# Performance work log

Measured on AMD Instinct MI355X. Metric: run time of the kernel, lower is better.

## Reference

```python
import jax, jax.numpy as jnp
import numpy as np

D_MODEL = 1024
NHEAD = 16
HEAD_DIM = D_MODEL // NHEAD
LN_EPS = 1e-5


def setup_inputs() -> dict:
    key = jax.random.key(0)
    ks = jax.random.split(key, 6)
    B, S = 4, 4096
    x = jax.random.normal(ks[0], (B, S, D_MODEL), dtype=jnp.float32)
    scale = 0.02
    Wq = jax.random.normal(ks[1], (D_MODEL, D_MODEL), dtype=jnp.float32) * scale
    Wv = jax.random.normal(ks[2], (D_MODEL, D_MODEL), dtype=jnp.float32) * scale
    Wo = jax.random.normal(ks[3], (D_MODEL, D_MODEL), dtype=jnp.float32) * scale
    Wg = jax.random.normal(ks[4], (D_MODEL, D_MODEL), dtype=jnp.float32) * scale
    beta = jnp.full((NHEAD,), -0.2, dtype=jnp.float32)
    ln_gamma = jnp.ones((D_MODEL,), dtype=jnp.float32)
    ln_beta = jnp.zeros((D_MODEL,), dtype=jnp.float32)
    return {"x": x, "Wq": Wq, "Wv": Wv, "Wo": Wo, "Wg": Wg,
            "beta": beta, "ln_gamma": ln_gamma, "ln_beta": ln_beta}


def _ema_scan(lam, v):
    # v: [B, S, H, D]; lam: [1, 1, H, 1]
    # s_t = lam * s_{t-1} + v_t, computed with a parallel associative scan
    # on pairs (a, b) representing the affine map s -> a*s + b.
    a = jnp.broadcast_to(lam, v.shape)

    def combine(e1, e2):
        a1, b1 = e1
        a2, b2 = e2
        return a1 * a2, a2 * b1 + b2

    _, state = jax.lax.associative_scan(combine, (a, v), axis=1)
    return state


def reference(x, Wq, Wv, Wo, Wg, beta, ln_gamma, ln_beta):
    B, S, _ = x.shape
    q = (x @ Wq.T).reshape(B, S, NHEAD, HEAD_DIM)
    v = (x @ Wv.T).reshape(B, S, NHEAD, HEAD_DIM)
    lam = jax.nn.sigmoid(beta).reshape(1, 1, NHEAD, 1).astype(v.dtype)
    state = _ema_scan(lam, v)                      # [B, S, H, D]
    y = (q * state).reshape(B, S, D_MODEL)
    # LayerNorm over last dim
    mu = jnp.mean(y, axis=-1, keepdims=True)
    var = jnp.mean(jnp.square(y - mu), axis=-1, keepdims=True)
    y = (y - mu) * jax.lax.rsqrt(var + LN_EPS) * ln_gamma + ln_beta
    gate = jax.nn.silu(x @ Wg.T)
    y = y * gate
    return y @ Wo.T
```

## Files before the change

kernel.cpp:

```cpp
#include <hip/hip_runtime.h>

#define D_MODEL 1024
#define NHEAD 16
#define LN_EPS 1e-5f
#define CHUNK 32
#define S_LEN 4096
#define NCH (S_LEN / CHUNK)

typedef unsigned short u16;
typedef __attribute__((ext_vector_type(8))) short short8;
typedef __attribute__((ext_vector_type(8))) unsigned short u16x8;
typedef __attribute__((ext_vector_type(4))) float f32x4;

__device__ __forceinline__ u16 f2b(float f) {
  unsigned u = __builtin_bit_cast(unsigned, f);
  u += 0x7FFFu + ((u >> 16) & 1u);
  return (u16)(u >> 16);
}
__device__ __forceinline__ float b2f(u16 s) {
  return __builtin_bit_cast(float, ((unsigned)s) << 16);
}

__device__ __forceinline__ ushort4 cvt4(float4 f) {
  ushort4 o; o.x = f2b(f.x); o.y = f2b(f.y); o.z = f2b(f.z); o.w = f2b(f.w);
  return o;
}
__global__ __launch_bounds__(256) void cvt_all(
    const float4* __restrict__ x,  const float4* __restrict__ wq,
    const float4* __restrict__ wv, const float4* __restrict__ wg,
    const float4* __restrict__ wo, ushort4* __restrict__ xb,
    ushort4* __restrict__ wqvg, ushort4* __restrict__ wob,
    const float* __restrict__ beta, float* __restrict__ lam,
    int nx4, int nw4) {
  int i = blockIdx.x * blockDim.x + threadIdx.x;
  int stride = gridDim.x * blockDim.x;
  if (blockIdx.x == 0 && threadIdx.x < NHEAD) {
    float l = 1.f / (1.f + __expf(-beta[threadIdx.x]));
    lam[threadIdx.x] = l;
    lam[NHEAD + threadIdx.x] = __log2f(l);
  }
  for (int j = i; j < nx4; j += stride) xb[j] = cvt4(x[j]);
  for (int j = i; j < nw4; j += stride) wqvg[j] = cvt4(wq[j]);
  for (int j = i; j < nw4; j += stride) wqvg[nw4 + j] = cvt4(wv[j]);
  for (int j = i; j < nw4; j += stride) wqvg[2 * nw4 + j] = cvt4(wg[j]);
  for (int j = i; j < nw4; j += stride) wob[j] = cvt4(wo[j]);
}


__device__ __forceinline__ void glds16(const u16* g, const u16* l) {
  __builtin_amdgcn_global_load_lds(
      (const __attribute__((address_space(1))) unsigned*)g,
      (__attribute__((address_space(3))) unsigned*)l, 16, 0, 0);
}

#define BAR() asm volatile("s_barrier" ::: "memory")
#define SB0() __builtin_amdgcn_sched_barrier(0)

template <typename OutT, bool CARRY>
__global__ __launch_bounds__(512, 2) void gemm256(const u16* __restrict__ X,
                                                  const u16* __restrict__ W,
                                                  OutT* __restrict__ Out,
                                                  float* __restrict__ carry,
                                                  const float* __restrict__ lamlog,
                                                  int M, int N, int K) {
  __shared__ u16 sm[8][8192];
  const int tid = threadIdx.x;
  const int lane = tid & 63;
  const int wave = tid >> 6;
  const int ln15 = lane & 15, lh = lane >> 4;
  const int wr = wave >> 2, wc = wave & 3;
  const int bm = blockIdx.x * 256, bn = blockIdx.y * 256;
  const int NT = K >> 6;

  const int srow = tid >> 3;
  const int scol = ((tid & 7) ^ (srow & 7)) << 3;
  const u16* Asrc = X + (size_t)(bm + srow) * K + scol;
  const u16* Bsrc = W + (size_t)(bn + srow) * K + scol;
  const int ldsw = wave * 512;

#define STAGE(u, h, tile, src)                                          \
  { const u16* _g = (src) + (size_t)((h) * 128) * K + (tile) * 64;      \
    glds16(_g,                  &sm[u][ldsw]);                          \
    glds16(_g + (size_t)64 * K, &sm[u][ldsw + 4096]); }

  const char* smb = (const char*)&sm[0][0];
  const char* Ard = smb + wr * 16384 + ln15 * 128;
  const char* Brd = smb + (2 + (wc >> 1)) * 16384 + ((wc & 1) * 64 + ln15) * 128;
  const int swz0 = ((lh ^ (ln15 & 7)) << 4);
  const int swz1 = (((4 + lh) ^ (ln15 & 7)) << 4);

#define RD_A(DB, MM, S) (*(const short8*)(Ard + (DB) + (MM) * 2048 + (S)))
#define RD_B(DB, NN, S) (*(const short8*)(Brd + (DB) + (NN) * 2048 + (S)))

  f32x4 acc[8][4];
  f32x4 zero = {0.f, 0.f, 0.f, 0.f};
  #pragma unroll
  for (int m = 0; m < 8; ++m)
    #pragma unroll
    for (int n = 0; n < 4; ++n) acc[m][n] = zero;

  short8 a[8][2], b[4][2];

#define MFMA_Q(M0, N0)                                                        \
  SB0();                                                                      \
  __builtin_amdgcn_s_setprio(1);                                              \
  _Pragma("unroll")                                                           \
  for (int m = (M0); m < (M0) + 4; ++m)                                       \
    _Pragma("unroll")                                                         \
    for (int n = (N0); n < (N0) + 2; ++n) {                                   \
      acc[m][n] = __builtin_amdgcn_mfma_f32_16x16x32_bf16(a[m][0], b[n][0], acc[m][n], 0, 0, 0); \
      acc[m][n] = __builtin_amdgcn_mfma_f32_16x16x32_bf16(a[m][1], b[n][1], acc[m][n], 0, 0, 0); \
    }                                                                         \
  __builtin_amdgcn_s_setprio(0);                                              \
  SB0();

  STAGE(0, 0, 0, Asrc); STAGE(1, 1, 0, Asrc);
  STAGE(2, 0, 0, Bsrc); STAGE(3, 1, 0, Bsrc);
  STAGE(4, 0, 1, Asrc); STAGE(5, 1, 1, Asrc);
  asm volatile("s_waitcnt vmcnt(4)" ::: "memory");
  BAR();
  #pragma unroll
  for (int m = 0; m < 4; ++m) { a[m][0] = RD_A(0, m, swz0); a[m][1] = RD_A(0, m, swz1); }
  #pragma unroll
  for (int n = 0; n < 4; ++n) { b[n][0] = RD_B(0, n, swz0); b[n][1] = RD_B(0, n, swz1); }

  for (int t = 0; t < NT; ++t) {
    const int d = t & 1;
    const int db = d * 65536;
    const int odb = (d ^ 1) * 65536;
    const int od = (d ^ 1) * 4;
    const int sd = d * 4;
    const int tB = (t + 1 < NT) ? t + 1 : NT - 1;
    const int tA = (t + 2 < NT) ? t + 2 : NT - 1;

    a[4][0] = RD_A(db, 4, swz0); a[4][1] = RD_A(db, 4, swz1);
    a[5][0] = RD_A(db, 5, swz0); a[5][1] = RD_A(db, 5, swz1);
    STAGE(od + 2, 0, tB, Bsrc);
    MFMA_Q(0, 0)

    a[6][0] = RD_A(db, 6, swz0); a[6][1] = RD_A(db, 6, swz1);
    a[7][0] = RD_A(db, 7, swz0); a[7][1] = RD_A(db, 7, swz1);
    STAGE(od + 3, 1, tB, Bsrc);
    MFMA_Q(0, 2)
    asm volatile("s_waitcnt vmcnt(4)" ::: "memory");
    BAR();

    #pragma unroll
    for (int m = 0; m < 4; ++m) { a[m][0] = RD_A(odb, m, swz0); a[m][1] = RD_A(odb, m, swz1); }
    MFMA_Q(4, 2)
    STAGE(sd + 0, 0, tA, Asrc);
    asm volatile("s_waitcnt vmcnt(2)" ::: "memory");
    BAR();

    b[2][0] = RD_B(odb, 2, swz0); b[2][1] = RD_B(odb, 2, swz1);
    b[3][0] = RD_B(odb, 3, swz0); b[3][1] = RD_B(odb, 3, swz1);
    MFMA_Q(4, 0)
    b[0][0] = RD_B(odb, 0, swz0); b[0][1] = RD_B(odb, 0, swz1);
    b[1][0] = RD_B(odb, 1, swz0); b[1][1] = RD_B(odb, 1, swz1);
    STAGE(sd + 1, 1, tA, Asrc);
  }
#undef STAGE
#undef RD_A
#undef RD_B
#undef MFMA_Q

  if constexpr (CARRY) {
    if (bn >= 1024 && bn < 2048) {
      const float l2h = lamlog[((bn - 1024) + wc * 64) >> 6];
      const float lp1 = exp2f(l2h);
      const float lp2 = lp1 * lp1, lp3 = lp2 * lp1, lp4 = lp2 * lp2;
      const float l8 = lp4 * lp4;
      const float lpl = exp2f(l2h * (float)(4 * lh));
      #pragma unroll
      for (int q = 0; q < 4; ++q)
        #pragma unroll
        for (int n = 0; n < 4; ++n) {
          f32x4 A0 = acc[2 * q][n], A1 = acc[2 * q + 1][n];
          A0[1] += lp1 * A0[0]; A0[2] += lp1 * A0[1]; A0[3] += lp1 * A0[2];
          A1[1] += lp1 * A1[0]; A1[2] += lp1 * A1[1]; A1[3] += lp1 * A1[2];
          float S = A0[3], x;
          x = __shfl_up(S, 16); if (lh >= 1) S += lp4 * x;
          x = __shfl_up(S, 32); if (lh >= 2) S += l8 * x;
          float Xc = __shfl_up(S, 16); Xc = (lh >= 1) ? Xc : 0.f;
          A0[0] += lp1 * Xc; A0[1] += lp2 * Xc; A0[2] += lp3 * Xc; A0[3] += lp4 * Xc;
          float f15 = __shfl(A0[3], 48 + ln15);
          S = A1[3];
          x = __shfl_up(S, 16); if (lh >= 1) S += lp4 * x;
          x = __shfl_up(S, 32); if (lh >= 2) S += l8 * x;
          Xc = __shfl_up(S, 16); Xc = (lh >= 1) ? Xc : 0.f;
          Xc += lpl * f15;
          A1[0] += lp1 * Xc; A1[1] += lp2 * Xc; A1[2] += lp3 * Xc; A1[3] += lp4 * Xc;
          acc[2 * q][n] = A0; acc[2 * q + 1][n] = A1;
        }
    }
  }

  #pragma unroll
  for (int m = 0; m < 8; ++m)
    #pragma unroll
    for (int n = 0; n < 4; ++n)
      #pragma unroll
      for (int r = 0; r < 4; ++r) {
        int row = bm + wr * 128 + m * 16 + lh * 4 + r;
        int col = bn + wc * 64 + n * 16 + ln15;
        float vv = acc[m][n][r];
        if constexpr (sizeof(OutT) == 2) Out[(size_t)row * N + col] = f2b(vv);
        else                             Out[(size_t)row * N + col] = vv;
      }

  if constexpr (CARRY) {
    if (bn >= 1024 && bn < 2048 && lh == 3) {
      const int bidx = bm >> 12;
      const int chunkbase = ((bm & 4095) >> 5) + wr * 4;
      const int colbase = (bn - 1024) + wc * 64;
      #pragma unroll
      for (int q = 0; q < 4; ++q)
        #pragma unroll
        for (int n = 0; n < 4; ++n)
          carry[(size_t)(bidx * NCH + chunkbase + q) * D_MODEL +
                colbase + n * 16 + ln15] = acc[2 * q + 1][n][3];
    }
  }
}

__global__ void scan_carry(float* __restrict__ carry, const float* __restrict__ lam,
                           int B, int nch) {
  int idx = blockIdx.x * blockDim.x + threadIdx.x;
  if (idx >= B * D_MODEL) return;
  int b = idx >> 10, col = idx & (D_MODEL - 1);
  float lC = exp2f(lam[NHEAD + (col >> 6)] * (float)CHUNK);
  float c = 0.f;
  #pragma unroll 4
  for (int j = 0; j < nch; ++j) {
    size_t a = ((size_t)(b * nch + j)) * D_MODEL + col;
    c = lC * c + carry[a];
    carry[a] = c;
  }
}

__global__ __launch_bounds__(256) void ew_ln(const u16* __restrict__ qvg,
    const float* __restrict__ carry, const float* __restrict__ lam,
    const float* __restrict__ gamma, const float* __restrict__ lbeta,
    u16* __restrict__ yout, int nch, int ld) {
  const int wave = threadIdx.x >> 6;
  const int lane = threadIdx.x & 63;
  const int row = blockIdx.x * 4 + wave;
  const int b = row >> 12;
  const int srow = row & 4095;
  const int j = srow >> 5, tl = srow & 31;
  const int col0 = lane * 16;
  const size_t rb = (size_t)row * ld;

  u16x8 qu0 = *(const u16x8*)(qvg + rb + col0);
  u16x8 qu1 = *(const u16x8*)(qvg + rb + col0 + 8);
  u16x8 su0 = *(const u16x8*)(qvg + rb + D_MODEL + col0);
  u16x8 su1 = *(const u16x8*)(qvg + rb + D_MODEL + col0 + 8);
  u16x8 gu0 = *(const u16x8*)(qvg + rb + 2 * D_MODEL + col0);
  u16x8 gu1 = *(const u16x8*)(qvg + rb + 2 * D_MODEL + col0 + 8);

  float st[16];
  #pragma unroll
  for (int i = 0; i < 8; ++i) { st[i] = b2f(su0[i]); st[8 + i] = b2f(su1[i]); }
  if (j > 0) {
    float p = exp2f(lam[NHEAD + (col0 >> 6)] * (float)(tl + 1));
    const float* cb = carry + ((size_t)(b * nch + j - 1)) * D_MODEL + col0;
    const float4 c0 = *(const float4*)(cb);
    const float4 c1 = *(const float4*)(cb + 4);
    const float4 c2 = *(const float4*)(cb + 8);
    const float4 c3 = *(const float4*)(cb + 12);
    st[0]  += p * c0.x; st[1]  += p * c0.y; st[2]  += p * c0.z; st[3]  += p * c0.w;
    st[4]  += p * c1.x; st[5]  += p * c1.y; st[6]  += p * c1.z; st[7]  += p * c1.w;
    st[8]  += p * c2.x; st[9]  += p * c2.y; st[10] += p * c2.z; st[11] += p * c2.w;
    st[12] += p * c3.x; st[13] += p * c3.y; st[14] += p * c3.z; st[15] += p * c3.w;
  }
  float y[16];
  float sum = 0.f, sumsq = 0.f;
  #pragma unroll
  for (int i = 0; i < 8; ++i) {
    y[i] = b2f(qu0[i]) * st[i];
    y[8 + i] = b2f(qu1[i]) * st[8 + i];
  }
  #pragma unroll
  for (int i = 0; i < 16; ++i) { sum += y[i]; sumsq += y[i] * y[i]; }
  #pragma unroll
  for (int off = 32; off > 0; off >>= 1) {
    sum += __shfl_xor(sum, off);
    sumsq += __shfl_xor(sumsq, off);
  }
  const float mu = sum * (1.f / 1024.f);
  const float var = sumsq * (1.f / 1024.f) - mu * mu;
  const float rstd = rsqrtf(var + LN_EPS);

  u16x8 o0, o1;
  #pragma unroll
  for (int i = 0; i < 8; ++i) {
    float gm = gamma[col0 + i], bt = lbeta[col0 + i];
    float g = b2f(gu0[i]);
    o0[i] = f2b(((y[i] - mu) * rstd * gm + bt) * (g / (1.f + __expf(-g))));
    gm = gamma[col0 + 8 + i]; bt = lbeta[col0 + 8 + i];
    g = b2f(gu1[i]);
    o1[i] = f2b(((y[8 + i] - mu) * rstd * gm + bt) * (g / (1.f + __expf(-g))));
  }
  *(u16x8*)(yout + (size_t)row * D_MODEL + col0) = o0;
  *(u16x8*)(yout + (size_t)row * D_MODEL + col0 + 8) = o1;
}

extern "C" void kernel_launch(void* const* d_in, const int* in_sizes, int n_in,
                              void* d_out, int out_size, void* d_ws, size_t ws_size,
                              hipStream_t stream) {
  const float* x     = (const float*)d_in[0];
  const float* Wq    = (const float*)d_in[1];
  const float* Wv    = (const float*)d_in[2];
  const float* Wo    = (const float*)d_in[3];
  const float* Wg    = (const float*)d_in[4];
  const float* beta  = (const float*)d_in[5];
  const float* gamma = (const float*)d_in[6];
  const float* lbeta = (const float*)d_in[7];
  float* out = (float*)d_out;

  const int BS = in_sizes[0] / D_MODEL;
  const int B = BS / S_LEN;
  const int nch = NCH;
  const size_t nx = (size_t)BS * D_MODEL;
  const size_t nw = (size_t)D_MODEL * D_MODEL;
  const int N3 = 3 * D_MODEL;

  char* w = (char*)d_ws;
  u16* xb   = (u16*)w;  w += nx * 2;
  u16* wqvg = (u16*)w;  w += 3 * nw * 2;
  u16* wob  = (u16*)w;  w += nw * 2;
  u16* qvg  = (u16*)w;  w += (size_t)BS * N3 * 2;
  u16* yb   = (u16*)w;  w += nx * 2;
  float* carry = (float*)w;  w += (size_t)B * nch * D_MODEL * 4;
  float* lam = (float*)w;

  cvt_all<<<2048, 256, 0, stream>>>((const float4*)x, (const float4*)Wq,
      (const float4*)Wv, (const float4*)Wg, (const float4*)Wo,
      (ushort4*)xb, (ushort4*)wqvg, (ushort4*)wob, beta, lam,
      (int)(nx / 4), (int)(nw / 4));

  dim3 g1(BS / 256, N3 / 256);
  gemm256<u16, true><<<g1, 512, 0, stream>>>(xb, wqvg, qvg, carry, lam + NHEAD,
                                             BS, N3, D_MODEL);

  scan_carry<<<(B * D_MODEL + 255) / 256, 256, 0, stream>>>(carry, lam, B, nch);
  ew_ln<<<BS / 4, 256, 0, stream>>>(qvg, carry, lam, gamma, lbeta, yb, nch, N3);

  dim3 g2(BS / 256, D_MODEL / 256);
  gemm256<float, false><<<g2, 512, 0, stream>>>(yb, wob, out, nullptr, nullptr,
                                                BS, D_MODEL, D_MODEL);
}
```

Baseline: 222.9 us.

## Load GEMM B operand directly from global into registers, halve LDS

The B (weight) tile is no longer staged through LDS. Each wave now reads its B fragments straight from global memory into double-buffered registers (bE/bO), and only the A tile is staged in LDS, which shrinks shared memory from 128KB to 64KB. The main loop is unrolled by two to alternate register buffers, and the waitcnt/barrier schedule is reworked to match. This removes LDS traffic and barriers for B and frees LDS for occupancy, at the cost of redundant uncoalesced global/L2 reads of B across waves and higher register pressure.

```diff
diff --git a/kernel.cpp b/kernel.cpp
--- a/kernel.cpp
+++ b/kernel.cpp
@@ -63,7 +63,7 @@
                                                   float* __restrict__ carry,
                                                   const float* __restrict__ lamlog,
                                                   int M, int N, int K) {
-  __shared__ u16 sm[8][8192];
+  __shared__ u16 sm[4][8192];
   const int tid = threadIdx.x;
   const int lane = tid & 63;
   const int wave = tid >> 6;
@@ -75,22 +75,27 @@
   const int srow = tid >> 3;
   const int scol = ((tid & 7) ^ (srow & 7)) << 3;
   const u16* Asrc = X + (size_t)(bm + srow) * K + scol;
-  const u16* Bsrc = W + (size_t)(bn + srow) * K + scol;
   const int ldsw = wave * 512;
 
-#define STAGE(u, h, tile, src)                                          \
-  { const u16* _g = (src) + (size_t)((h) * 128) * K + (tile) * 64;      \
+#define STAGE_A(u, h, tile)                                             \
+  { const u16* _g = Asrc + (size_t)((h) * 128) * K + (tile) * 64;       \
     glds16(_g,                  &sm[u][ldsw]);                          \
     glds16(_g + (size_t)64 * K, &sm[u][ldsw + 4096]); }
 
+  const u16* Bgl = W + (size_t)(bn + wc * 64 + ln15) * K + lh * 8;
+#define LOADB(BV, tile)                                                 \
+  _Pragma("unroll")                                                     \
+  for (int n = 0; n < 4; ++n) {                                         \
+    BV[n][0] = *(const short8*)(Bgl + (size_t)n * 16 * K + (tile) * 64);      \
+    BV[n][1] = *(const short8*)(Bgl + (size_t)n * 16 * K + (tile) * 64 + 32); \
+  }
+
   const char* smb = (const char*)&sm[0][0];
   const char* Ard = smb + wr * 16384 + ln15 * 128;
-  const char* Brd = smb + (2 + (wc >> 1)) * 16384 + ((wc & 1) * 64 + ln15) * 128;
   const int swz0 = ((lh ^ (ln15 & 7)) << 4);
   const int swz1 = (((4 + lh) ^ (ln15 & 7)) << 4);
 
 #define RD_A(DB, MM, S) (*(const short8*)(Ard + (DB) + (MM) * 2048 + (S)))
-#define RD_B(DB, NN, S) (*(const short8*)(Brd + (DB) + (NN) * 2048 + (S)))
 
   f32x4 acc[8][4];
   f32x4 zero = {0.f, 0.f, 0.f, 0.f};
@@ -99,69 +104,73 @@
     #pragma unroll
     for (int n = 0; n < 4; ++n) acc[m][n] = zero;
 
-  short8 a[8][2], b[4][2];
-
-#define MFMA_Q(M0, N0)                                                        \
+  short8 a[8][2], bE[4][2], bO[4][2];
+
+#define MFMA_Q(M0, N0, BV)                                                    \
   SB0();                                                                      \
   __builtin_amdgcn_s_setprio(1);                                              \
   _Pragma("unroll")                                                           \
   for (int m = (M0); m < (M0) + 4; ++m)                                       \
     _Pragma("unroll")                                                         \
     for (int n = (N0); n < (N0) + 2; ++n) {                                   \
-      acc[m][n] = __builtin_amdgcn_mfma_f32_16x16x32_bf16(a[m][0], b[n][0], acc[m][n], 0, 0, 0); \
-      acc[m][n] = __builtin_amdgcn_mfma_f32_16x16x32_bf16(a[m][1], b[n][1], acc[m][n], 0, 0, 0); \
+      acc[m][n] = __builtin_amdgcn_mfma_f32_16x16x32_bf16(a[m][0], BV[n][0], acc[m][n], 0, 0, 0); \
+      acc[m][n] = __builtin_amdgcn_mfma_f32_16x16x32_bf16(a[m][1], BV[n][1], acc[m][n], 0, 0, 0); \
     }                                                                         \
   __builtin_amdgcn_s_setprio(0);                                              \
   SB0();
 
-  STAGE(0, 0, 0, Asrc); STAGE(1, 1, 0, Asrc);
-  STAGE(2, 0, 0, Bsrc); STAGE(3, 1, 0, Bsrc);
-  STAGE(4, 0, 1, Asrc); STAGE(5, 1, 1, Asrc);
+  LOADB(bE, 0)
+  STAGE_A(0, 0, 0) STAGE_A(1, 1, 0)
+  STAGE_A(2, 0, 1) STAGE_A(3, 1, 1)
   asm volatile("s_waitcnt vmcnt(4)" ::: "memory");
   BAR();
   #pragma unroll
   for (int m = 0; m < 4; ++m) { a[m][0] = RD_A(0, m, swz0); a[m][1] = RD_A(0, m, swz1); }
-  #pragma unroll
-  for (int n = 0; n < 4; ++n) { b[n][0] = RD_B(0, n, swz0); b[n][1] = RD_B(0, n, swz1); }
-
-  for (int t = 0; t < NT; ++t) {
-    const int d = t & 1;
-    const int db = d * 65536;
-    const int odb = (d ^ 1) * 65536;
-    const int od = (d ^ 1) * 4;
-    const int sd = d * 4;
-    const int tB = (t + 1 < NT) ? t + 1 : NT - 1;
-    const int tA = (t + 2 < NT) ? t + 2 : NT - 1;
-
-    a[4][0] = RD_A(db, 4, swz0); a[4][1] = RD_A(db, 4, swz1);
-    a[5][0] = RD_A(db, 5, swz0); a[5][1] = RD_A(db, 5, swz1);
-    STAGE(od + 2, 0, tB, Bsrc);
-    MFMA_Q(0, 0)
-
-    a[6][0] = RD_A(db, 6, swz0); a[6][1] = RD_A(db, 6, swz1);
-    a[7][0] = RD_A(db, 7, swz0); a[7][1] = RD_A(db, 7, swz1);
-    STAGE(od + 3, 1, tB, Bsrc);
-    MFMA_Q(0, 2)
-    asm volatile("s_waitcnt vmcnt(4)" ::: "memory");
+
+  for (int i = 0; i < NT / 2; ++i) {
+    const int T = 2 * i;
+    const int tb0 = (T + 1 < NT) ? T + 1 : NT - 1;
+    const int ta0 = (T + 2 < NT) ? T + 2 : NT - 1;
+    const int tb1 = (T + 2 < NT) ? T + 2 : NT - 1;
+    const int ta1 = (T + 3 < NT) ? T + 3 : NT - 1;
+
+    LOADB(bO, tb0)
+    a[4][0] = RD_A(0, 4, swz0); a[4][1] = RD_A(0, 4, swz1);
+    a[5][0] = RD_A(0, 5, swz0); a[5][1] = RD_A(0, 5, swz1);
+    MFMA_Q(0, 0, bE)
+    a[6][0] = RD_A(0, 6, swz0); a[6][1] = RD_A(0, 6, swz1);
+    a[7][0] = RD_A(0, 7, swz0); a[7][1] = RD_A(0, 7, swz1);
+    MFMA_Q(0, 2, bE)
+    asm volatile("s_waitcnt vmcnt(8)" ::: "memory");
     BAR();
-
     #pragma unroll
-    for (int m = 0; m < 4; ++m) { a[m][0] = RD_A(odb, m, swz0); a[m][1] = RD_A(odb, m, swz1); }
-    MFMA_Q(4, 2)
-    STAGE(sd + 0, 0, tA, Asrc);
-    asm volatile("s_waitcnt vmcnt(2)" ::: "memory");
+    for (int m = 0; m < 4; ++m) { a[m][0] = RD_A(32768, m, swz0); a[m][1] = RD_A(32768, m, swz1); }
+    MFMA_Q(4, 2, bE)
+    STAGE_A(0, 0, ta0)
+    MFMA_Q(4, 0, bE)
+    STAGE_A(1, 1, ta0)
     BAR();
 
-    b[2][0] = RD_B(odb, 2, swz0); b[2][1] = RD_B(odb, 2, swz1);
-    b[3][0] = RD_B(odb, 3, swz0); b[3][1] = RD_B(odb, 3, swz1);
-    MFMA_Q(4, 0)
-    b[0][0] = RD_B(odb, 0, swz0); b[0][1] = RD_B(odb, 0, swz1);
-    b[1][0] = RD_B(odb, 1, swz0); b[1][1] = RD_B(odb, 1, swz1);
-    STAGE(sd + 1, 1, tA, Asrc);
-  }
-#undef STAGE
+    LOADB(bE, tb1)
+    a[4][0] = RD_A(32768, 4, swz0); a[4][1] = RD_A(32768, 4, swz1);
+    a[5][0] = RD_A(32768, 5, swz0); a[5][1] = RD_A(32768, 5, swz1);
+    MFMA_Q(0, 0, bO)
+    a[6][0] = RD_A(32768, 6, swz0); a[6][1] = RD_A(32768, 6, swz1);
+    a[7][0] = RD_A(32768, 7, swz0); a[7][1] = RD_A(32768, 7, swz1);
+    MFMA_Q(0, 2, bO)
+    asm volatile("s_waitcnt vmcnt(8)" ::: "memory");
+    BAR();
+    #pragma unroll
+    for (int m = 0; m < 4; ++m) { a[m][0] = RD_A(0, m, swz0); a[m][1] = RD_A(0, m, swz1); }
+    MFMA_Q(4, 2, bO)
+    STAGE_A(2, 0, ta1)
+    MFMA_Q(4, 0, bO)
+    STAGE_A(3, 1, ta1)
+    BAR();
+  }
+#undef STAGE_A
+#undef LOADB
 #undef RD_A
-#undef RD_B
 #undef MFMA_Q
 
   if constexpr (CARRY) {
```

New measurement: 435.6 us. +95.4%, slower.
